# Kernel tuning notes

Hardware: AMD Instinct MI355X
Metric: run time of the kernel (lower is better)

Reference implementation:

```python
import jax, jax.numpy as jnp
import numpy as np

H = 256  # hidden_dim
N = 100000  # num nodes in local_embedding
U = 65536  # num unary clauses
B = 65536  # num binary clauses


def setup_inputs() -> dict:
    key = jax.random.key(0)
    ks = jax.random.split(key, 20)
    s = 0.02
    inp = {
        "local_embedding": jax.random.normal(ks[0], (N, H), dtype=jnp.float32),
        "global_embedding": jax.random.normal(ks[1], (1, H), dtype=jnp.float32),
        "unary_idx": jax.random.randint(ks[2], (U, 2), 0, N, dtype=jnp.int64),
        "binary_idx": jax.random.randint(ks[3], (B, 3), 0, N, dtype=jnp.int64),
        # binary_op_layer: Linear(3H,2H) -> ReLU -> Linear(2H,H)
        "Wb1": jax.random.normal(ks[4], (3 * H, 2 * H), dtype=jnp.float32) * s,
        "bb1": jnp.zeros((2 * H,), dtype=jnp.float32),
        "Wb2": jax.random.normal(ks[5], (2 * H, H), dtype=jnp.float32) * s,
        "bb2": jnp.zeros((H,), dtype=jnp.float32),
        # ternary_op_layer: Linear(4H,2H) -> ReLU -> Linear(2H,H)
        "Wt1": jax.random.normal(ks[6], (4 * H, 2 * H), dtype=jnp.float32) * s,
        "bt1": jnp.zeros((2 * H,), dtype=jnp.float32),
        "Wt2": jax.random.normal(ks[7], (2 * H, H), dtype=jnp.float32) * s,
        "bt2": jnp.zeros((H,), dtype=jnp.float32),
        # common_layer: ReLU -> Linear(H,H) -> ReLU -> Linear(H,1)
        "Wc1": jax.random.normal(ks[8], (H, H), dtype=jnp.float32) * s,
        "bc1": jnp.zeros((H,), dtype=jnp.float32),
        "Wc2": jax.random.normal(ks[9], (H, 1), dtype=jnp.float32) * s,
        "bc2": jnp.zeros((1,), dtype=jnp.float32),
    }
    return inp


def _mlp_branch(rep, W1, b1, W2, b2, Wc1, bc1, Wc2, bc2):
    # op layer: Linear -> ReLU -> Linear
    h = jax.nn.relu(rep @ W1 + b1) @ W2 + b2  # [M, H]
    # common layer: ReLU -> Linear -> ReLU -> Linear(H,1)
    h = jax.nn.relu(jax.nn.relu(h) @ Wc1 + bc1) @ Wc2 + bc2  # [M, 1]
    return h[:, 0]


def reference(local_embedding, global_embedding, unary_idx, binary_idx,
              Wb1, bb1, Wb2, bb2, Wt1, bt1, Wt2, bt2, Wc1, bc1, Wc2, bc2):
    u = unary_idx.shape[0]
    b = binary_idx.shape[0]
    h = global_embedding.shape[-1]
    # gather [U,2,H] node embeddings, append global -> [U,3,H] -> [U,3H]
    g_u = jnp.broadcast_to(global_embedding[None, :, :], (u, 1, h))
    unary_rep = jnp.concatenate(
        (local_embedding[unary_idx, :], g_u), axis=1).reshape(u, 3 * h)
    x_u = _mlp_branch(unary_rep, Wb1, bb1, Wb2, bb2, Wc1, bc1, Wc2, bc2)
    # gather [B,3,H], append global -> [B,4,H] -> [B,4H]
    g_b = jnp.broadcast_to(global_embedding[None, :, :], (b, 1, h))
    binary_rep = jnp.concatenate(
        (local_embedding[binary_idx, :], g_b), axis=1).reshape(b, 4 * h)
    x_b = _mlp_branch(binary_rep, Wt1, bt1, Wt2, bt2, Wc1, bc1, Wc2, bc2)
    x = jnp.concatenate((x_u, x_b))
    return x.reshape(1, x.shape[-1])
```

## Files before the change

### kernel.cpp

```cpp
#include <hip/hip_runtime.h>
#include <cstdint>
#include <cstddef>

typedef __attribute__((ext_vector_type(8))) short s16x8;
typedef __attribute__((ext_vector_type(4))) float fx4;

#define AS1 __attribute__((address_space(1)))
#define AS3 __attribute__((address_space(3)))

__device__ __forceinline__ unsigned short f2bf(float f) {
    union { float f; unsigned u; } c; c.f = f;
    unsigned lsb = (c.u >> 16) & 1u;
    unsigned r = c.u + 0x7fffu + lsb;
    return (unsigned short)(r >> 16);
}

__device__ __forceinline__ void ctj(const float* __restrict__ W,
                                    unsigned short* __restrict__ WT,
                                    int K, int N, int brel, int tid) {
    int i = brel * 256 + tid;
    int n = i / K, k = i - n * K;
    WT[i] = f2bf(W[(size_t)k * N + n]);
}

__global__ __launch_bounds__(256) void prep(
    const float* __restrict__ emb, unsigned short* __restrict__ emb_bf,
    int n4, int NB1,
    const float* __restrict__ Wb1, unsigned short* __restrict__ W1uT,
    const float* __restrict__ Wb2, unsigned short* __restrict__ W2uT,
    const float* __restrict__ Wt1, unsigned short* __restrict__ W1bT,
    const float* __restrict__ Wt2, unsigned short* __restrict__ W2bT,
    const float* __restrict__ Wc1, unsigned short* __restrict__ Wc1T,
    const float* __restrict__ g, const float* __restrict__ bb1,
    const float* __restrict__ bt1,
    float* __restrict__ bu, float* __restrict__ bbn) {
    int bid = blockIdx.x, tid = threadIdx.x;
    if (bid < NB1) {
        int i = bid * 256 + tid;
        if (i < n4) {
            float4 v = reinterpret_cast<const float4*>(emb)[i];
            ushort4 o;
            o.x = f2bf(v.x); o.y = f2bf(v.y); o.z = f2bf(v.z); o.w = f2bf(v.w);
            reinterpret_cast<ushort4*>(emb_bf)[i] = o;
        }
        return;
    }
    int b2 = bid - NB1;
    if (b2 < 3840) {
        if (b2 < 1024)      ctj(Wb1, W1uT, 512, 512, b2, tid);
        else if (b2 < 1536) ctj(Wb2, W2uT, 512, 256, b2 - 1024, tid);
        else if (b2 < 3072) ctj(Wt1, W1bT, 768, 512, b2 - 1536, tid);
        else if (b2 < 3584) ctj(Wt2, W2bT, 512, 256, b2 - 3072, tid);
        else                ctj(Wc1, Wc1T, 256, 256, b2 - 3584, tid);
        return;
    }
    int b3 = b2 - 3840;
    int wv = tid >> 6, lane = tid & 63;
    int col = b3 * 4 + wv;
    const float* W  = (col < 512) ? Wb1 : Wt1;
    const float* bs = (col < 512) ? bb1 : bt1;
    float* dst      = (col < 512) ? bu  : bbn;
    int K0          = (col < 512) ? 512 : 768;
    int n = col & 511;
    float s = 0.f;
#pragma unroll
    for (int j = 0; j < 4; ++j) {
        int k = lane + j * 64;
        s += g[k] * W[(size_t)(K0 + k) * 512 + n];
    }
#pragma unroll
    for (int off = 32; off > 0; off >>= 1) s += __shfl_xor(s, off, 64);
    if (lane == 0) dst[n] = bs[n] + s;
}


#define GLL(src, dst) __builtin_amdgcn_global_load_lds((AS1 void*)(src), (AS3 void*)(dst), 16, 0, 0)

#define MFMA16(mh, nh, BARR) do { \
    _Pragma("unroll") for (int ks_ = 0; ks_ < 2; ++ks_) \
    _Pragma("unroll") for (int r_ = 0; r_ < 4; ++r_) \
    _Pragma("unroll") for (int c_ = 0; c_ < 2; ++c_) \
        acc[(mh) * 4 + r_][(nh) * 2 + c_] = __builtin_amdgcn_mfma_f32_16x16x32_bf16( \
            a[r_ * 2 + ks_], BARR[c_ * 2 + ks_], acc[(mh) * 4 + r_][(nh) * 2 + c_], 0, 0, 0); \
} while (0)

#define SYNC_PRE() do { \
    __builtin_amdgcn_s_barrier(); \
    asm volatile("s_waitcnt lgkmcnt(0)" ::: "memory"); \
    __builtin_amdgcn_sched_barrier(0); \
    __builtin_amdgcn_s_setprio(1); \
} while (0)

#define READ_A_AT(basep, mh) do { \
    const char* base_ = (basep); \
    _Pragma("unroll") for (int r_ = 0; r_ < 4; ++r_) { \
        a[r_ * 2 + 0] = *(const s16x8*)(base_ + ((mh) * 4 + r_) * 2048 + c0); \
        a[r_ * 2 + 1] = *(const s16x8*)(base_ + ((mh) * 4 + r_) * 2048 + c1); \
    } \
} while (0)

#define READ_B_AT(basep, nh, BARR) do { \
    const char* base_ = (basep); \
    _Pragma("unroll") for (int c_ = 0; c_ < 2; ++c_) { \
        BARR[c_ * 2 + 0] = *(const s16x8*)(base_ + ((nh) * 2 + c_) * 2048 + c0); \
        BARR[c_ * 2 + 1] = *(const s16x8*)(base_ + ((nh) * 2 + c_) * 2048 + c1); \
    } \
} while (0)

template <int MODE, int K, int NODES>
__global__ __launch_bounds__(512, 2) void gemm256(
    const unsigned short* __restrict__ Abase,
    const int* __restrict__ idx,
    const unsigned short* __restrict__ WT,
    const float* __restrict__ bias,
    unsigned short* __restrict__ Hout,
    int N, int nbn) {
    __shared__ alignas(16) char smem_c[131072];
    constexpr int KT = K / 64;

    const int t = threadIdx.x;
    const int w = t >> 6, lane = t & 63;
    const int wm = w >> 2, wn = w & 3;

    const int nwg = gridDim.x, o = blockIdx.x, q = nwg >> 3;
    const int widx = (o & 7) * q + (o >> 3);
    const int bn = widx % nbn, bm = widx / nbn;

    const int l3 = lane >> 3, l7 = lane & 7, l15 = lane & 15;
    const int scs = (l7 ^ l3) << 4;

    const char* Abc = (const char*)Abase;
    const char* WTc = (const char*)WT;

    uint32_t boff[2][2];
    uint32_t aoff[2][2][NODES];
#pragma unroll
    for (int h = 0; h < 2; ++h)
#pragma unroll
        for (int r = 0; r < 2; ++r) {
            int srow = h * 128 + w * 8 + l3 + r * 64;
            boff[h][r] = (uint32_t)(bn * 256 + srow) * (uint32_t)(K * 2) + scs;
            int gm = bm * 256 + srow;
            if constexpr (MODE == 0) {
                aoff[h][r][0] = (uint32_t)gm * (uint32_t)(K * 2) + scs;
            } else {
#pragma unroll
                for (int s = 0; s < NODES; ++s)
                    aoff[h][r][s] = (uint32_t)idx[(size_t)gm * NODES + s] * 512u + scs;
            }
        }

#define STAGE_A(hh, tsrc, pb) do { \
    char* d_ = smem_c + (pb) * 65536 + (hh) * 16384 + (w << 10); \
    if constexpr (MODE == 0) { \
        GLL(Abc + aoff[hh][0][0] + (tsrc) * 128, d_); \
        GLL(Abc + aoff[hh][1][0] + (tsrc) * 128, d_ + 8192); \
    } else { \
        int seg_ = (tsrc) >> 2, k4_ = ((tsrc) & 3) << 7; \
        uint32_t v0_ = aoff[hh][0][0], v1_ = aoff[hh][1][0]; \
        if constexpr (NODES >= 2) { if (seg_ >= 1) { v0_ = aoff[hh][0][1]; v1_ = aoff[hh][1][1]; } } \
        if constexpr (NODES >= 3) { if (seg_ >= 2) { v0_ = aoff[hh][0][2]; v1_ = aoff[hh][1][2]; } } \
        GLL(Abc + v0_ + k4_, d_); GLL(Abc + v1_ + k4_, d_ + 8192); \
    } \
} while (0)

#define STAGE_B(hh, tsrc, pb) do { \
    char* d_ = smem_c + (pb) * 65536 + 32768 + (hh) * 16384 + (w << 10); \
    GLL(WTc + boff[hh][0] + (tsrc) * 128, d_); \
    GLL(WTc + boff[hh][1] + (tsrc) * 128, d_ + 8192); \
} while (0)

    const int armul = wm * 16384 + l15 * 128;
    const int brmul = 32768 + wn * 8192 + l15 * 128;
    const int hi = (lane >> 4) << 4, xl = l7 << 4;
    const int c0 = hi ^ xl, c1 = (64 + hi) ^ xl;

    fx4 acc[8][4];
#pragma unroll
    for (int i = 0; i < 8; ++i)
#pragma unroll
        for (int j = 0; j < 4; ++j) acc[i][j] = {0.f, 0.f, 0.f, 0.f};

    STAGE_A(0, 0, 0); STAGE_A(1, 0, 0); STAGE_B(0, 0, 0); STAGE_B(1, 0, 0);
    STAGE_A(0, 1, 1);
    asm volatile("s_waitcnt vmcnt(2)" ::: "memory");
    __builtin_amdgcn_s_barrier();

    s16x8 a[8], bl[4], bh[4];
    for (int tt = 0; tt < KT; tt += 2) {
        const int t1 = tt + 1;
        const int t2c = (tt + 2 < KT) ? tt + 2 : KT - 1;
        const int t3c = (tt + 3 < KT) ? tt + 3 : KT - 1;

        READ_A_AT(smem_c + armul, 0); READ_B_AT(smem_c + brmul, 0, bl);
        STAGE_A(1, t1, 1);
        SYNC_PRE(); MFMA16(0, 0, bl); __builtin_amdgcn_s_setprio(0);
        __builtin_amdgcn_s_barrier();

        READ_B_AT(smem_c + brmul, 1, bh);
        STAGE_B(0, t1, 1);
        SYNC_PRE(); MFMA16(0, 1, bh); __builtin_amdgcn_s_setprio(0);
        __builtin_amdgcn_s_barrier();

        READ_A_AT(smem_c + armul, 1);
        STAGE_B(1, t1, 1);
        SYNC_PRE(); MFMA16(1, 0, bl); __builtin_amdgcn_s_setprio(0);
        __builtin_amdgcn_s_barrier();

        STAGE_A(0, t2c, 0);
        SYNC_PRE(); MFMA16(1, 1, bh); __builtin_amdgcn_s_setprio(0);
        asm volatile("s_waitcnt vmcnt(2)" ::: "memory");
        __builtin_amdgcn_s_barrier();

        READ_A_AT(smem_c + 65536 + armul, 0); READ_B_AT(smem_c + 65536 + brmul, 0, bl);
        STAGE_A(1, t2c, 0);
        SYNC_PRE(); MFMA16(0, 0, bl); __builtin_amdgcn_s_setprio(0);
        __builtin_amdgcn_s_barrier();

        READ_B_AT(smem_c + 65536 + brmul, 1, bh);
        STAGE_B(0, t2c, 0);
        SYNC_PRE(); MFMA16(0, 1, bh); __builtin_amdgcn_s_setprio(0);
        __builtin_amdgcn_s_barrier();

        READ_A_AT(smem_c + 65536 + armul, 1);
        STAGE_B(1, t2c, 0);
        SYNC_PRE(); MFMA16(1, 0, bl); __builtin_amdgcn_s_setprio(0);
        __builtin_amdgcn_s_barrier();

        STAGE_A(0, t3c, 1);
        SYNC_PRE(); MFMA16(1, 1, bh); __builtin_amdgcn_s_setprio(0);
        asm volatile("s_waitcnt vmcnt(2)" ::: "memory");
        __builtin_amdgcn_s_barrier();
    }
    asm volatile("s_waitcnt vmcnt(0)" ::: "memory");
#undef STAGE_A
#undef STAGE_B

    const int hi2 = (lane >> 4);
#pragma unroll
    for (int mi = 0; mi < 8; ++mi) {
#pragma unroll
        for (int ni = 0; ni < 4; ++ni) {
            int gcol = bn * 256 + wn * 64 + ni * 16 + l15;
            float bvv = bias[gcol];
            int grow0 = bm * 256 + wm * 128 + mi * 16 + hi2 * 4;
            fx4 v = acc[mi][ni];
#pragma unroll
            for (int j = 0; j < 4; ++j) {
                float x = fmaxf(v[j] + bvv, 0.f);
                Hout[(size_t)(grow0 + j) * N + gcol] = f2bf(x);
            }
        }
    }
}

__global__ __launch_bounds__(512, 2) void gemm_tail(
    const unsigned short* __restrict__ h1u,
    const unsigned short* __restrict__ h1b,
    const unsigned short* __restrict__ W2uT,
    const unsigned short* __restrict__ W2bT,
    const float* __restrict__ bb2,
    const float* __restrict__ bt2,
    const unsigned short* __restrict__ Wc1T,
    const float* __restrict__ bc1,
    const float* __restrict__ Wc2,
    const float* __restrict__ bc2,
    float* __restrict__ outF, int U) {
    __shared__ alignas(16) char smem_c[163840];
    constexpr int K = 512, KT = K / 64;

    const int t = threadIdx.x;
    const int w = t >> 6, lane = t & 63;
    const int wm = w >> 2, wn = w & 3;
    const int br = blockIdx.x & 1;
    const int bm = blockIdx.x >> 1;

    const unsigned short* h1  = br ? h1b : h1u;
    const unsigned short* W2T = br ? W2bT : W2uT;
    const float* bias2        = br ? bt2 : bb2;
    float* outp               = outF + br * U;

    const int l3 = lane >> 3, l7 = lane & 7, l15 = lane & 15;
    const int scs = (l7 ^ l3) << 4;

    const char* Abc = (const char*)h1;
    const char* WTc = (const char*)W2T;
    const char* Wc1c = (const char*)Wc1T;

    uint32_t boff[2][2], aoff[2][2];
#pragma unroll
    for (int h = 0; h < 2; ++h)
#pragma unroll
        for (int r = 0; r < 2; ++r) {
            int srow = h * 128 + w * 8 + l3 + r * 64;
            boff[h][r] = (uint32_t)srow * (uint32_t)(K * 2) + scs;
            aoff[h][r] = (uint32_t)(bm * 256 + srow) * (uint32_t)(K * 2) + scs;
        }

    uint32_t p2src[2], p2dst[2];
#pragma unroll
    for (int p = 0; p < 2; ++p) {
        int o = p * 8192 + t * 16;
        int l = o >> 7, u = (o >> 4) & 7;
        int ulog = u ^ (l & 7);
        int r = 2 * l + (ulog >> 2), gg = ulog & 3;
        p2src[p] = (uint32_t)r * 512u + (uint32_t)gg * 16u;
        p2dst[p] = (uint32_t)o;
    }

#define TSTAGE_A(hh, tsrc, pb) do { \
    char* d_ = smem_c + (pb) * 65536 + (hh) * 16384 + (w << 10); \
    GLL(Abc + aoff[hh][0] + (tsrc) * 128, d_); \
    GLL(Abc + aoff[hh][1] + (tsrc) * 128, d_ + 8192); \
} while (0)

#define TSTAGE_B(hh, tsrc, pb) do { \
    char* d_ = smem_c + (pb) * 65536 + 32768 + (hh) * 16384 + (w << 10); \
    GLL(WTc + boff[hh][0] + (tsrc) * 128, d_); \
    GLL(WTc + boff[hh][1] + (tsrc) * 128, d_ + 8192); \
} while (0)

#define STAGE2(kt, buf) do { \
    char* d_ = smem_c + 131072 + (buf) * 16384; \
    GLL(Wc1c + p2src[0] + (kt) * 64, d_ + p2dst[0]); \
    GLL(Wc1c + p2src[1] + (kt) * 64, d_ + p2dst[1]); \
} while (0)

    const int armul = wm * 16384 + l15 * 128;
    const int brmul = 32768 + wn * 8192 + l15 * 128;
    const int hi = (lane >> 4) << 4, xl = l7 << 4;
    const int c0 = hi ^ xl, c1 = (64 + hi) ^ xl;

    fx4 acc[8][4];
#pragma unroll
    for (int i = 0; i < 8; ++i)
#pragma unroll
        for (int j = 0; j < 4; ++j) acc[i][j] = {0.f, 0.f, 0.f, 0.f};

    TSTAGE_A(0, 0, 0); TSTAGE_A(1, 0, 0); TSTAGE_B(0, 0, 0); TSTAGE_B(1, 0, 0);
    TSTAGE_A(0, 1, 1);
    asm volatile("s_waitcnt vmcnt(2)" ::: "memory");
    __builtin_amdgcn_s_barrier();

    s16x8 a[8], bl[4], bh[4];
    for (int tt = 0; tt < KT; tt += 2) {
        const int t1 = tt + 1;
        const int t2c = (tt + 2 < KT) ? tt + 2 : KT - 1;
        const int t3c = (tt + 3 < KT) ? tt + 3 : KT - 1;

        READ_A_AT(smem_c + armul, 0); READ_B_AT(smem_c + brmul, 0, bl);
        TSTAGE_A(1, t1, 1);
        SYNC_PRE(); MFMA16(0, 0, bl); __builtin_amdgcn_s_setprio(0);
        __builtin_amdgcn_s_barrier();

        READ_B_AT(smem_c + brmul, 1, bh);
        TSTAGE_B(0, t1, 1);
        SYNC_PRE(); MFMA16(0, 1, bh); __builtin_amdgcn_s_setprio(0);
        __builtin_amdgcn_s_barrier();

        READ_A_AT(smem_c + armul, 1);
        TSTAGE_B(1, t1, 1);
        SYNC_PRE(); MFMA16(1, 0, bl); __builtin_amdgcn_s_setprio(0);
        __builtin_amdgcn_s_barrier();

        TSTAGE_A(0, t2c, 0);
        SYNC_PRE(); MFMA16(1, 1, bh); __builtin_amdgcn_s_setprio(0);
        asm volatile("s_waitcnt vmcnt(2)" ::: "memory");
        __builtin_amdgcn_s_barrier();

        READ_A_AT(smem_c + 65536 + armul, 0); READ_B_AT(smem_c + 65536 + brmul, 0, bl);
        TSTAGE_A(1, t2c, 0);
        SYNC_PRE(); MFMA16(0, 0, bl); __builtin_amdgcn_s_setprio(0);
        __builtin_amdgcn_s_barrier();

        READ_B_AT(smem_c + 65536 + brmul, 1, bh);
        TSTAGE_B(0, t2c, 0);
        SYNC_PRE(); MFMA16(0, 1, bh); __builtin_amdgcn_s_setprio(0);
        __builtin_amdgcn_s_barrier();

        READ_A_AT(smem_c + 65536 + armul, 1);
        TSTAGE_B(1, t2c, 0);
        SYNC_PRE(); MFMA16(1, 0, bl); __builtin_amdgcn_s_setprio(0);
        __builtin_amdgcn_s_barrier();

        TSTAGE_A(0, t3c, 1);
        SYNC_PRE(); MFMA16(1, 1, bh); __builtin_amdgcn_s_setprio(0);
        asm volatile("s_waitcnt vmcnt(2)" ::: "memory");
        __builtin_amdgcn_s_barrier();
    }
    asm volatile("s_waitcnt vmcnt(0)" ::: "memory");
#undef TSTAGE_A
#undef TSTAGE_B

    STAGE2(0, 0); STAGE2(1, 1);

    __syncthreads();
    const int hi2 = (lane >> 4);
    {
        float b2v[4];
#pragma unroll
        for (int ni = 0; ni < 4; ++ni) b2v[ni] = bias2[wn * 64 + ni * 16 + l15];
#pragma unroll
        for (int mi = 0; mi < 8; ++mi) {
#pragma unroll
            for (int ni = 0; ni < 4; ++ni) {
                int kin2 = (ni * 16 + l15) * 2;
                fx4 v = acc[mi][ni];
#pragma unroll
                for (int j = 0; j < 4; ++j) {
                    int row = wm * 128 + mi * 16 + hi2 * 4 + j;
                    int byte = wn * 32768 + row * 128 + (kin2 ^ ((row & 7) << 4));
                    *(unsigned short*)(smem_c + byte) =
                        f2bf(fmaxf(v[j] + b2v[ni], 0.f));
                }
            }
        }
    }
#pragma unroll
    for (int i = 0; i < 8; ++i)
#pragma unroll
        for (int j = 0; j < 4; ++j) acc[i][j] = {0.f, 0.f, 0.f, 0.f};
    __syncthreads();

    const int g2 = lane >> 4;
    for (int kt = 0; kt < 8; ++kt) {
        if (kt < 7) { asm volatile("s_waitcnt vmcnt(2)" ::: "memory"); }
        else        { asm volatile("s_waitcnt vmcnt(0)" ::: "memory"); }
        __builtin_amdgcn_s_barrier();

        s16x8 a2[8], b2f[4];
        const int kc = kt >> 1, half = kt & 1;
        const int cb = half * 64 + (g2 << 4);
        const char* ab = smem_c + kc * 32768;
#pragma unroll
        for (int m = 0; m < 8; ++m) {
            int row = wm * 128 + m * 16 + l15;
            a2[m] = *(const s16x8*)(ab + row * 128 + (cb ^ ((row & 7) << 4)));
        }
        const char* bb = smem_c + 131072 + (kt & 1) * 16384;
#pragma unroll
        for (int f = 0; f < 4; ++f) {
            int r = wn * 64 + f * 16 + l15;
            int l = r >> 1;
            int u = (((r & 1) << 2) | g2) ^ (l & 7);
            b2f[f] = *(const s16x8*)(bb + l * 128 + u * 16);
        }
        asm volatile("s_waitcnt lgkmcnt(0)" ::: "memory");
        __builtin_amdgcn_sched_barrier(0);
        __builtin_amdgcn_s_barrier();
        if (kt + 2 < 8) STAGE2(kt + 2, kt & 1);
        __builtin_amdgcn_s_setprio(1);
#pragma unroll
        for (int m = 0; m < 8; ++m)
#pragma unroll
            for (int f = 0; f < 4; ++f)
                acc[m][f] = __builtin_amdgcn_mfma_f32_16x16x32_bf16(
                    a2[m], b2f[f], acc[m][f], 0, 0, 0);
        __builtin_amdgcn_s_setprio(0);
    }
#undef STAGE2

    float* part = (float*)(smem_c + 131072);
    float bv[4], wv[4];
#pragma unroll
    for (int ni = 0; ni < 4; ++ni) {
        int gcol = wn * 64 + ni * 16 + l15;
        bv[ni] = bc1[gcol];
        wv[ni] = Wc2[gcol];
    }
#pragma unroll
    for (int mi = 0; mi < 8; ++mi) {
#pragma unroll
        for (int j = 0; j < 4; ++j) {
            float s = 0.f;
#pragma unroll
            for (int ni = 0; ni < 4; ++ni)
                s += fmaxf(acc[mi][ni][j] + bv[ni], 0.f) * wv[ni];
            s += __shfl_xor(s, 1); s += __shfl_xor(s, 2);
            s += __shfl_xor(s, 4); s += __shfl_xor(s, 8);
            if (l15 == 0) {
                int row = wm * 128 + mi * 16 + hi2 * 4 + j;
                part[row * 4 + wn] = s;
            }
        }
    }
    __syncthreads();
    if (t < 256) {
        float o2 = part[t * 4] + part[t * 4 + 1] + part[t * 4 + 2] + part[t * 4 + 3] + bc2[0];
        outp[bm * 256 + t] = o2;
    }
}

extern "C" void kernel_launch(void* const* d_in, const int* in_sizes, int n_in,
                              void* d_out, int out_size, void* d_ws, size_t ws_size,
                              hipStream_t stream) {
    const float* local_emb  = (const float*)d_in[0];
    const float* global_emb = (const float*)d_in[1];
    const int* unary_idx    = (const int*)d_in[2];
    const int* binary_idx   = (const int*)d_in[3];
    const float* Wb1 = (const float*)d_in[4];
    const float* bb1 = (const float*)d_in[5];
    const float* Wb2 = (const float*)d_in[6];
    const float* bb2 = (const float*)d_in[7];
    const float* Wt1 = (const float*)d_in[8];
    const float* bt1 = (const float*)d_in[9];
    const float* Wt2 = (const float*)d_in[10];
    const float* bt2 = (const float*)d_in[11];
    const float* Wc1 = (const float*)d_in[12];
    const float* bc1 = (const float*)d_in[13];
    const float* Wc2 = (const float*)d_in[14];
    const float* bc2 = (const float*)d_in[15];
    float* out = (float*)d_out;

    constexpr int Hd = 256, U = 65536;
    const int NN = in_sizes[0] / Hd;

    char* ws = (char*)d_ws;
    size_t off = 0;
    auto alloc = [&](size_t bytes) {
        char* p = ws + off;
        off += (bytes + 255) & ~(size_t)255;
        return p;
    };
    unsigned short* emb_bf = (unsigned short*)alloc((size_t)NN * Hd * 2);
    unsigned short* W1uT   = (unsigned short*)alloc(512 * 512 * 2);
    unsigned short* W2uT   = (unsigned short*)alloc(256 * 512 * 2);
    unsigned short* W1bT   = (unsigned short*)alloc(512 * 768 * 2);
    unsigned short* W2bT   = (unsigned short*)alloc(256 * 512 * 2);
    unsigned short* Wc1T   = (unsigned short*)alloc(256 * 256 * 2);
    float* bu              = (float*)alloc(512 * 4);
    float* bbn             = (float*)alloc(512 * 4);
    unsigned short* h1u    = (unsigned short*)alloc((size_t)U * 512 * 2);
    unsigned short* h1b    = (unsigned short*)alloc((size_t)U * 512 * 2);

    int n4 = NN * 64;
    int NB1 = (n4 + 255) / 256;
    prep<<<dim3(NB1 + 3840 + 256), dim3(256), 0, stream>>>(
        local_emb, emb_bf, n4, NB1,
        Wb1, W1uT, Wb2, W2uT, Wt1, W1bT, Wt2, W2bT, Wc1, Wc1T,
        global_emb, bb1, bt1, bu, bbn);

    dim3 blk(512);
    gemm256<1, 512, 2><<<dim3(512), blk, 0, stream>>>(
        emb_bf, unary_idx, W1uT, bu, h1u, 512, 2);
    gemm256<2, 768, 3><<<dim3(512), blk, 0, stream>>>(
        emb_bf, binary_idx, W1bT, bbn, h1b, 512, 2);
    gemm_tail<<<dim3(512), blk, 0, stream>>>(
        h1u, h1b, W2uT, W2bT, bb2, bt2, Wc1T, bc1, Wc2, bc2, out, U);

    (void)n_in; (void)out_size; (void)ws_size;
}
```

Before: 218.8 us.

## Merge unary/binary first-layer GEMMs into one launch; load Wc1 directly to registers

The two templated first-layer GEMM launches become a single 1024-block kernel that picks the unary or binary branch per block, with runtime K and node count. This removes a launch boundary and the tail-effect idle time between the two grids. In the tail kernel, the Wc1 tiles are now read straight from global memory into registers with double buffering, replacing the LDS-staged, barrier-synchronised pipeline, and the LDS allocation shrinks. The cost is runtime branching and a loop trip count that is no longer a compile-time constant in the first GEMM, and possibly more register pressure and global-load latency in the tail.

```diff
diff --git a/kernel.cpp b/kernel.cpp
--- a/kernel.cpp
+++ b/kernel.cpp
@@ -107,16 +107,13 @@
     } \
 } while (0)
 
-template <int MODE, int K, int NODES>
-__global__ __launch_bounds__(512, 2) void gemm256(
-    const unsigned short* __restrict__ Abase,
-    const int* __restrict__ idx,
-    const unsigned short* __restrict__ WT,
-    const float* __restrict__ bias,
-    unsigned short* __restrict__ Hout,
-    int N, int nbn) {
+__global__ __launch_bounds__(512, 2) void gemm256_dual(
+    const unsigned short* __restrict__ emb,
+    const int* __restrict__ uidx, const int* __restrict__ bidx,
+    const unsigned short* __restrict__ W1uT, const unsigned short* __restrict__ W1bT,
+    const float* __restrict__ bu, const float* __restrict__ bbn,
+    unsigned short* __restrict__ h1u, unsigned short* __restrict__ h1b) {
     __shared__ alignas(16) char smem_c[131072];
-    constexpr int KT = K / 64;
 
     const int t = threadIdx.x;
     const int w = t >> 6, lane = t & 63;
@@ -124,44 +121,45 @@
 
     const int nwg = gridDim.x, o = blockIdx.x, q = nwg >> 3;
     const int widx = (o & 7) * q + (o >> 3);
-    const int bn = widx % nbn, bm = widx / nbn;
+    const int bn = widx & 1, br = (widx >> 1) & 1, bm = widx >> 2;
+
+    const int KT = 8 + 4 * br;
+    const int K2 = (512 + 256 * br) * 2;
+    const int nodes = 2 + br;
+    const int* idx = br ? bidx : uidx;
+    const unsigned short* WT = br ? W1bT : W1uT;
+    const float* bias = br ? bbn : bu;
+    unsigned short* Hout = br ? h1b : h1u;
 
     const int l3 = lane >> 3, l7 = lane & 7, l15 = lane & 15;
     const int scs = (l7 ^ l3) << 4;
 
-    const char* Abc = (const char*)Abase;
+    const char* Abc = (const char*)emb;
     const char* WTc = (const char*)WT;
 
     uint32_t boff[2][2];
-    uint32_t aoff[2][2][NODES];
+    uint32_t aoff[2][2][3];
 #pragma unroll
     for (int h = 0; h < 2; ++h)
 #pragma unroll
         for (int r = 0; r < 2; ++r) {
             int srow = h * 128 + w * 8 + l3 + r * 64;
-            boff[h][r] = (uint32_t)(bn * 256 + srow) * (uint32_t)(K * 2) + scs;
+            boff[h][r] = (uint32_t)(bn * 256 + srow) * (uint32_t)K2 + scs;
             int gm = bm * 256 + srow;
-            if constexpr (MODE == 0) {
-                aoff[h][r][0] = (uint32_t)gm * (uint32_t)(K * 2) + scs;
-            } else {
-#pragma unroll
-                for (int s = 0; s < NODES; ++s)
-                    aoff[h][r][s] = (uint32_t)idx[(size_t)gm * NODES + s] * 512u + scs;
-            }
+            const int* ip = idx + (size_t)gm * nodes;
+            int n0 = ip[0], n1 = ip[1], n2 = br ? ip[2] : ip[0];
+            aoff[h][r][0] = (uint32_t)n0 * 512u + scs;
+            aoff[h][r][1] = (uint32_t)n1 * 512u + scs;
+            aoff[h][r][2] = (uint32_t)n2 * 512u + scs;
         }
 
 #define STAGE_A(hh, tsrc, pb) do { \
     char* d_ = smem_c + (pb) * 65536 + (hh) * 16384 + (w << 10); \
-    if constexpr (MODE == 0) { \
-        GLL(Abc + aoff[hh][0][0] + (tsrc) * 128, d_); \
-        GLL(Abc + aoff[hh][1][0] + (tsrc) * 128, d_ + 8192); \
-    } else { \
-        int seg_ = (tsrc) >> 2, k4_ = ((tsrc) & 3) << 7; \
-        uint32_t v0_ = aoff[hh][0][0], v1_ = aoff[hh][1][0]; \
-        if constexpr (NODES >= 2) { if (seg_ >= 1) { v0_ = aoff[hh][0][1]; v1_ = aoff[hh][1][1]; } } \
-        if constexpr (NODES >= 3) { if (seg_ >= 2) { v0_ = aoff[hh][0][2]; v1_ = aoff[hh][1][2]; } } \
-        GLL(Abc + v0_ + k4_, d_); GLL(Abc + v1_ + k4_, d_ + 8192); \
-    } \
+    int seg_ = (tsrc) >> 2, k4_ = ((tsrc) & 3) << 7; \
+    uint32_t v0_ = aoff[hh][0][0], v1_ = aoff[hh][1][0]; \
+    if (seg_ >= 1) { v0_ = aoff[hh][0][1]; v1_ = aoff[hh][1][1]; } \
+    if (seg_ >= 2) { v0_ = aoff[hh][0][2]; v1_ = aoff[hh][1][2]; } \
+    GLL(Abc + v0_ + k4_, d_); GLL(Abc + v1_ + k4_, d_ + 8192); \
 } while (0)
 
 #define STAGE_B(hh, tsrc, pb) do { \
@@ -248,7 +246,7 @@
 #pragma unroll
             for (int j = 0; j < 4; ++j) {
                 float x = fmaxf(v[j] + bvv, 0.f);
-                Hout[(size_t)(grow0 + j) * N + gcol] = f2bf(x);
+                Hout[(size_t)(grow0 + j) * 512 + gcol] = f2bf(x);
             }
         }
     }
@@ -266,7 +264,7 @@
     const float* __restrict__ Wc2,
     const float* __restrict__ bc2,
     float* __restrict__ outF, int U) {
-    __shared__ alignas(16) char smem_c[163840];
+    __shared__ alignas(16) char smem_c[135168];
     constexpr int K = 512, KT = K / 64;
 
     const int t = threadIdx.x;
@@ -297,17 +295,6 @@
             aoff[h][r] = (uint32_t)(bm * 256 + srow) * (uint32_t)(K * 2) + scs;
         }
 
-    uint32_t p2src[2], p2dst[2];
-#pragma unroll
-    for (int p = 0; p < 2; ++p) {
-        int o = p * 8192 + t * 16;
-        int l = o >> 7, u = (o >> 4) & 7;
-        int ulog = u ^ (l & 7);
-        int r = 2 * l + (ulog >> 2), gg = ulog & 3;
-        p2src[p] = (uint32_t)r * 512u + (uint32_t)gg * 16u;
-        p2dst[p] = (uint32_t)o;
-    }
-
 #define TSTAGE_A(hh, tsrc, pb) do { \
     char* d_ = smem_c + (pb) * 65536 + (hh) * 16384 + (w << 10); \
     GLL(Abc + aoff[hh][0] + (tsrc) * 128, d_); \
@@ -318,12 +305,6 @@
     char* d_ = smem_c + (pb) * 65536 + 32768 + (hh) * 16384 + (w << 10); \
     GLL(WTc + boff[hh][0] + (tsrc) * 128, d_); \
     GLL(WTc + boff[hh][1] + (tsrc) * 128, d_ + 8192); \
-} while (0)
-
-#define STAGE2(kt, buf) do { \
-    char* d_ = smem_c + 131072 + (buf) * 16384; \
-    GLL(Wc1c + p2src[0] + (kt) * 64, d_ + p2dst[0]); \
-    GLL(Wc1c + p2src[1] + (kt) * 64, d_ + p2dst[1]); \
 } while (0)
 
     const int armul = wm * 16384 + l15 * 128;
@@ -392,7 +373,29 @@
 #undef TSTAGE_A
 #undef TSTAGE_B
 
-    STAGE2(0, 0); STAGE2(1, 1);
+    const char* wbase = Wc1c + (uint32_t)(wn * 64 + l15) * 512u + ((lane >> 4) << 4);
+#define LOADB(BUF, kt) do { \
+    _Pragma("unroll") for (int f_ = 0; f_ < 4; ++f_) \
+        BUF[f_] = *(const s16x8*)(wbase + f_ * 8192 + (kt) * 64); \
+} while (0)
+
+#define COMPUTE2(kt, BB) do { \
+    s16x8 a2_[8]; \
+    const char* ab_ = smem_c + ((kt) >> 1) * 32768; \
+    const int cb_ = ((kt) & 1) * 64 + ((lane >> 4) << 4); \
+    _Pragma("unroll") for (int m_ = 0; m_ < 8; ++m_) { \
+        int row_ = wm * 128 + m_ * 16 + l15; \
+        a2_[m_] = *(const s16x8*)(ab_ + row_ * 128 + (cb_ ^ ((row_ & 7) << 4))); \
+    } \
+    _Pragma("unroll") for (int m_ = 0; m_ < 8; ++m_) \
+    _Pragma("unroll") for (int f_ = 0; f_ < 4; ++f_) \
+        acc[m_][f_] = __builtin_amdgcn_mfma_f32_16x16x32_bf16( \
+            a2_[m_], BB[f_], acc[m_][f_], 0, 0, 0); \
+} while (0)
+
+    s16x8 b2a[4], b2b[4];
+    LOADB(b2a, 0); LOADB(b2b, 1);
+    __builtin_amdgcn_sched_barrier(0);
 
     __syncthreads();
     const int hi2 = (lane >> 4);
@@ -422,43 +425,15 @@
         for (int j = 0; j < 4; ++j) acc[i][j] = {0.f, 0.f, 0.f, 0.f};
     __syncthreads();
 
-    const int g2 = lane >> 4;
-    for (int kt = 0; kt < 8; ++kt) {
-        if (kt < 7) { asm volatile("s_waitcnt vmcnt(2)" ::: "memory"); }
-        else        { asm volatile("s_waitcnt vmcnt(0)" ::: "memory"); }
-        __builtin_amdgcn_s_barrier();
-
-        s16x8 a2[8], b2f[4];
-        const int kc = kt >> 1, half = kt & 1;
-        const int cb = half * 64 + (g2 << 4);
-        const char* ab = smem_c + kc * 32768;
-#pragma unroll
-        for (int m = 0; m < 8; ++m) {
-            int row = wm * 128 + m * 16 + l15;
-            a2[m] = *(const s16x8*)(ab + row * 128 + (cb ^ ((row & 7) << 4)));
-        }
-        const char* bb = smem_c + 131072 + (kt & 1) * 16384;
-#pragma unroll
-        for (int f = 0; f < 4; ++f) {
-            int r = wn * 64 + f * 16 + l15;
-            int l = r >> 1;
-            int u = (((r & 1) << 2) | g2) ^ (l & 7);
-            b2f[f] = *(const s16x8*)(bb + l * 128 + u * 16);
-        }
-        asm volatile("s_waitcnt lgkmcnt(0)" ::: "memory");
-        __builtin_amdgcn_sched_barrier(0);
-        __builtin_amdgcn_s_barrier();
-        if (kt + 2 < 8) STAGE2(kt + 2, kt & 1);
-        __builtin_amdgcn_s_setprio(1);
-#pragma unroll
-        for (int m = 0; m < 8; ++m)
-#pragma unroll
-            for (int f = 0; f < 4; ++f)
-                acc[m][f] = __builtin_amdgcn_mfma_f32_16x16x32_bf16(
-                    a2[m], b2f[f], acc[m][f], 0, 0, 0);
-        __builtin_amdgcn_s_setprio(0);
-    }
-#undef STAGE2
+#pragma unroll
+    for (int kp = 0; kp < 4; ++kp) {
+        COMPUTE2(2 * kp, b2a);
+        if (kp < 3) LOADB(b2a, 2 * kp + 2);
+        COMPUTE2(2 * kp + 1, b2b);
+        if (kp < 3) LOADB(b2b, 2 * kp + 3);
+    }
+#undef LOADB
+#undef COMPUTE2
 
     float* part = (float*)(smem_c + 131072);
     float bv[4], wv[4];
@@ -541,10 +516,8 @@
         global_emb, bb1, bt1, bu, bbn);
 
     dim3 blk(512);
-    gemm256<1, 512, 2><<<dim3(512), blk, 0, stream>>>(
-        emb_bf, unary_idx, W1uT, bu, h1u, 512, 2);
-    gemm256<2, 768, 3><<<dim3(512), blk, 0, stream>>>(
-        emb_bf, binary_idx, W1bT, bbn, h1b, 512, 2);
+    gemm256_dual<<<dim3(1024), blk, 0, stream>>>(
+        emb_bf, unary_idx, binary_idx, W1uT, W1bT, bu, bbn, h1u, h1b);
     gemm_tail<<<dim3(512), blk, 0, stream>>>(
         h1u, h1b, W2uT, W2bT, bb2, bt2, Wc1T, bc1, Wc2, bc2, out, U);
 
```

New measurement: 222.5 us. No clear change (+1.7%).
